# Performance work log

Hardware: AMD Instinct MI355X
Metric: run time of the kernel (lower is better)

The kernel has to match this reference:

```python
import jax, jax.numpy as jnp
import numpy as np

# segment-boundary byte set (matches ByteContextEncoder.SEGMENT_BYTES)
_SEG_BYTES = b' \t\n\r.,;:!?()[]{}"\'' + b'+-*/=<>|&^~%@#$\\'
_SEP_TABLE = np.zeros(256, dtype=bool)
_SEP_TABLE[list(_SEG_BYTES)] = True

B, T, D, H, L = 4, 2048, 512, 8, 4
HID = 4 * D          # SwiGLU hidden dim
DH = D // H          # head dim
EPS = 1e-6
ALPHA = 0.5
ROPE_BASE = 10000.0


def setup_inputs() -> dict:
    key = jax.random.key(0)
    ks = jax.random.split(key, 10)
    std = D ** -0.5
    tokens = jax.random.randint(ks[0], (B, T), 0, 256)
    embed = jax.random.normal(ks[1], (256, D), dtype=jnp.float32) * std
    wq = jax.random.normal(ks[2], (L, D, D), dtype=jnp.float32) * std
    wk = jax.random.normal(ks[3], (L, D, D), dtype=jnp.float32) * std
    wv = jax.random.normal(ks[4], (L, D, D), dtype=jnp.float32) * std
    wo = jax.random.normal(ks[5], (L, D, D), dtype=jnp.float32) * std
    w1 = jax.random.normal(ks[6], (L, HID, D), dtype=jnp.float32) * std  # gate proj
    w3 = jax.random.normal(ks[7], (L, HID, D), dtype=jnp.float32) * std  # up proj
    w2 = jax.random.normal(ks[8], (L, D, HID), dtype=jnp.float32) * (HID ** -0.5)  # down proj
    attn_norm_w = jnp.ones((L, D), dtype=jnp.float32)
    ffn_norm_w = jnp.ones((L, D), dtype=jnp.float32)
    final_norm_w = jnp.ones((D,), dtype=jnp.float32)
    return {"tokens": tokens, "embed": embed, "attn_norm_w": attn_norm_w,
            "wq": wq, "wk": wk, "wv": wv, "wo": wo,
            "ffn_norm_w": ffn_norm_w, "w1": w1, "w2": w2, "w3": w3,
            "final_norm_w": final_norm_w}


def _rmsnorm(x, w):
    return x * jax.lax.rsqrt(jnp.mean(x * x, axis=-1, keepdims=True) + EPS) * w


def _rope_tables():
    inv = 1.0 / (ROPE_BASE ** (jnp.arange(0, DH, 2, dtype=jnp.float32) / DH))  # (DH/2,)
    ang = jnp.arange(T, dtype=jnp.float32)[:, None] * inv[None, :]             # (T, DH/2)
    return jnp.cos(ang), jnp.sin(ang)


def _apply_rope(x, cos, sin):
    # x: (B, T, H, DH); rotate interleaved pairs
    x1, x2 = x[..., ::2], x[..., 1::2]
    c = cos[None, :, None, :]
    s = sin[None, :, None, :]
    r1 = x1 * c - x2 * s
    r2 = x1 * s + x2 * c
    return jnp.stack([r1, r2], axis=-1).reshape(x.shape)


def _attention(x, Wq, Wk, Wv, Wo, cos, sin):
    q = (x @ Wq.T).reshape(B, T, H, DH)
    k = (x @ Wk.T).reshape(B, T, H, DH)
    v = (x @ Wv.T).reshape(B, T, H, DH)
    q = _apply_rope(q, cos, sin)
    k = _apply_rope(k, cos, sin)
    scores = jnp.einsum('bthd,bshd->bhts', q, k) / jnp.sqrt(jnp.float32(DH))
    a = jax.nn.softmax(scores, axis=-1)  # bidirectional (causal=False)
    o = jnp.einsum('bhts,bshd->bthd', a, v).reshape(B, T, D)
    return o @ Wo.T


def _swiglu(x, W1, W2, W3):
    return (jax.nn.silu(x @ W1.T) * (x @ W3.T)) @ W2.T


def _segment_pool(h, tokens):
    # segment ids via cumsum of separator indicator; per-batch offset b*(T+1)
    sep = jnp.asarray(_SEP_TABLE)[tokens].astype(jnp.int32)          # (B, T)
    seg = jnp.cumsum(sep, axis=1) + jnp.arange(B, dtype=jnp.int32)[:, None] * (T + 1)
    flat_s = seg.reshape(B * T)
    flat_h = h.reshape(B * T, D)
    nseg = B * (T + 1)
    seg_sum = jax.ops.segment_sum(flat_h, flat_s, num_segments=nseg)  # (nseg, D)
    seg_cnt = jax.ops.segment_sum(jnp.ones((B * T,), h.dtype), flat_s, num_segments=nseg)
    seg_cnt = jnp.maximum(seg_cnt, 1.0)
    seg_mean = (seg_sum / seg_cnt[:, None])[flat_s].reshape(B, T, D)
    return ALPHA * h + (1.0 - ALPHA) * seg_mean


def reference(tokens, embed, attn_norm_w, wq, wk, wv, wo, ffn_norm_w, w1, w2, w3, final_norm_w):
    tokens = jnp.clip(tokens, 0, 255)
    x = embed[tokens]  # (B, T, D); dropout=0 -> identity
    cos, sin = _rope_tables()
    for l in range(L):
        x = x + _attention(_rmsnorm(x, attn_norm_w[l]), wq[l], wk[l], wv[l], wo[l], cos, sin)
        x = x + _swiglu(_rmsnorm(x, ffn_norm_w[l]), w1[l], w2[l], w3[l])
    x = _rmsnorm(x, final_norm_w)
    return _segment_pool(x, tokens)
```

## Files before the change

kernel.cpp:

```cpp
#include <hip/hip_runtime.h>
#include <math.h>

#define Bq 4
#define Tt 2048
#define Dd 512
#define Hh 8
#define Ll 4
#define HIDN 2048
#define DHd 64
#define BT (Bq*Tt)
#define BTD ((size_t)BT*Dd)

typedef __attribute__((ext_vector_type(8))) __bf16 bf16x8;
typedef __attribute__((ext_vector_type(4))) __bf16 bf16x4;
typedef __attribute__((ext_vector_type(2))) __bf16 bf16x2;
typedef __attribute__((ext_vector_type(4))) float f32x4;

static __device__ __forceinline__ int is_sep(int t) {
    const unsigned long long w0 = 0xFC00FFFF00002600ULL;
    const unsigned long long w1 = 0x7800000078000001ULL;
    if (t < 64)  return (int)((w0 >> t) & 1ULL);
    if (t < 128) return (int)((w1 >> (t - 64)) & 1ULL);
    return 0;
}

static __device__ __forceinline__ void gload16(const void* g, void* l) {
    __builtin_amdgcn_global_load_lds(
        (const __attribute__((address_space(1))) void*)g,
        (__attribute__((address_space(3))) void*)l, 16, 0, 0);
}

__global__ void embed_kernel(const int* __restrict__ tokens, const float* __restrict__ embed,
                             float* __restrict__ x) {
    size_t idx = (size_t)blockIdx.x * blockDim.x + threadIdx.x;
    if (idx >= BTD / 4) return;
    size_t row = idx >> 7;
    int tk = tokens[row];
    tk = tk < 0 ? 0 : (tk > 255 ? 255 : tk);
    const float4* src = (const float4*)(embed + (size_t)tk * Dd);
    ((float4*)x)[idx] = src[idx & 127];
}

__global__ void rope_table_kernel(float* __restrict__ cosb, float* __restrict__ sinb) {
    int idx = blockIdx.x * blockDim.x + threadIdx.x;
    if (idx >= Tt * 32) return;
    int t = idx >> 5, j = idx & 31;
    float inv = powf(10000.0f, -(2.0f * j) / 64.0f);
    float ang = (float)t * inv;
    cosb[idx] = cosf(ang);
    sinb[idx] = sinf(ang);
}

__global__ void cvt_bf16_kernel(const float* __restrict__ in, __bf16* __restrict__ out, int n8) {
    int i = blockIdx.x * blockDim.x + threadIdx.x;
    if (i >= n8) return;
    const float4* p = (const float4*)(in + (size_t)i * 8);
    float4 a = p[0], b = p[1];
    bf16x8 o8;
    o8[0] = (__bf16)a.x; o8[1] = (__bf16)a.y; o8[2] = (__bf16)a.z; o8[3] = (__bf16)a.w;
    o8[4] = (__bf16)b.x; o8[5] = (__bf16)b.y; o8[6] = (__bf16)b.z; o8[7] = (__bf16)b.w;
    *(bf16x8*)(out + (size_t)i * 8) = o8;
}

__global__ void cvt_qkv_kernel(const float* __restrict__ wq, const float* __restrict__ wk,
                               const float* __restrict__ wv, __bf16* __restrict__ out) {
    int i = blockIdx.x * blockDim.x + threadIdx.x;
    if (i >= 393216) return;
    int l = i / 98304;
    int r = i - l * 98304;
    int t = r >> 15;
    int pos8 = r & 32767;
    const float* src = (t == 0 ? wq : (t == 1 ? wk : wv)) + (size_t)l * 262144 + (size_t)pos8 * 8;
    float4 a = *(const float4*)src;
    float4 b = *(const float4*)(src + 4);
    bf16x8 o8;
    o8[0] = (__bf16)a.x; o8[1] = (__bf16)a.y; o8[2] = (__bf16)a.z; o8[3] = (__bf16)a.w;
    o8[4] = (__bf16)b.x; o8[5] = (__bf16)b.y; o8[6] = (__bf16)b.z; o8[7] = (__bf16)b.w;
    *(bf16x8*)(out + (size_t)i * 8) = o8;
}

__global__ void rmsnorm_kernel(const float* __restrict__ x, const float* __restrict__ w,
                               float* __restrict__ y) {
    int row = blockIdx.x * 4 + (threadIdx.x >> 6);
    int lane = threadIdx.x & 63;
    const float* xr = x + (size_t)row * Dd + lane * 8;
    float4 a = *(const float4*)xr;
    float4 b = *(const float4*)(xr + 4);
    float ss = a.x * a.x + a.y * a.y + a.z * a.z + a.w * a.w
             + b.x * b.x + b.y * b.y + b.z * b.z + b.w * b.w;
    #pragma unroll
    for (int off = 1; off < 64; off <<= 1) ss += __shfl_xor(ss, off);
    float scale = rsqrtf(ss * (1.0f / Dd) + 1e-6f);
    const float* wr = w + lane * 8;
    float4 wa = *(const float4*)wr;
    float4 wb = *(const float4*)(wr + 4);
    float* yo = y + (size_t)row * Dd + lane * 8;
    *(float4*)yo = make_float4(a.x * scale * wa.x, a.y * scale * wa.y,
                               a.z * scale * wa.z, a.w * scale * wa.w);
    *(float4*)(yo + 4) = make_float4(b.x * scale * wb.x, b.y * scale * wb.y,
                                     b.z * scale * wb.z, b.w * scale * wb.w);
}

__global__ void rmsnorm_bf16_kernel(const float* __restrict__ x, const float* __restrict__ w,
                                    __bf16* __restrict__ y) {
    int row = blockIdx.x * 4 + (threadIdx.x >> 6);
    int lane = threadIdx.x & 63;
    const float* xr = x + (size_t)row * Dd + lane * 8;
    float4 a = *(const float4*)xr;
    float4 b = *(const float4*)(xr + 4);
    float ss = a.x * a.x + a.y * a.y + a.z * a.z + a.w * a.w
             + b.x * b.x + b.y * b.y + b.z * b.z + b.w * b.w;
    #pragma unroll
    for (int off = 1; off < 64; off <<= 1) ss += __shfl_xor(ss, off);
    float scale = rsqrtf(ss * (1.0f / Dd) + 1e-6f);
    const float* wr = w + lane * 8;
    float4 wa = *(const float4*)wr;
    float4 wb = *(const float4*)(wr + 4);
    bf16x8 o;
    o[0] = (__bf16)(a.x * scale * wa.x); o[1] = (__bf16)(a.y * scale * wa.y);
    o[2] = (__bf16)(a.z * scale * wa.z); o[3] = (__bf16)(a.w * scale * wa.w);
    o[4] = (__bf16)(b.x * scale * wb.x); o[5] = (__bf16)(b.y * scale * wb.y);
    o[6] = (__bf16)(b.z * scale * wb.z); o[7] = (__bf16)(b.w * scale * wb.w);
    *(bf16x8*)(y + (size_t)row * Dd + lane * 8) = o;
}

template<int EPI>
__global__ __launch_bounds__(256) void gemm_bt_mfma(
    const __bf16* __restrict__ A, const __bf16* __restrict__ Bw,
    const float* __restrict__ res, void* __restrict__ Cout,
    int N, int K,
    const float* __restrict__ cosb, const float* __restrict__ sinb) {
    __shared__ __align__(16) __bf16 lds[2][2][128 * 32];
    const int tid = threadIdx.x;
    const int w = tid >> 6, lane = tid & 63;
    const int l15 = lane & 15, g4 = lane >> 4;
    const int wr = w >> 1, wc = w & 1;
    const int bm = blockIdx.y * 128, bn = blockIdx.x * 128;
    const int lrow = lane >> 2, lc8 = (lane & 3) * 8;
    const int chunk0 = w * 2;

    f32x4 acc[4][4];
    #pragma unroll
    for (int m = 0; m < 4; m++)
        #pragma unroll
        for (int n = 0; n < 4; n++) acc[m][n] = (f32x4){0.f, 0.f, 0.f, 0.f};

    auto stage = [&](int buf, int k0) {
        #pragma unroll
        for (int c = 0; c < 2; c++) {
            int chunk = chunk0 + c;
            const __bf16* ga = A + (size_t)(bm + chunk * 16 + lrow) * K + k0 + lc8;
            gload16(ga, &lds[buf][0][chunk * 512]);
            const __bf16* gb = Bw + (size_t)(bn + chunk * 16 + lrow) * K + k0 + lc8;
            gload16(gb, &lds[buf][1][chunk * 512]);
        }
    };

    stage(0, 0);
    __syncthreads();
    const int NT = K >> 5;
    int cur = 0;
    for (int t = 0; t < NT; t++) {
        if (t + 1 < NT) stage(cur ^ 1, (t + 1) << 5);
        const __bf16* Al = &lds[cur][0][0];
        const __bf16* Bl = &lds[cur][1][0];
        bf16x8 af[4], bfr[4];
        #pragma unroll
        for (int m = 0; m < 4; m++)
            af[m] = *(const bf16x8*)&Al[(wr * 64 + m * 16 + l15) * 32 + g4 * 8];
        #pragma unroll
        for (int n = 0; n < 4; n++)
            bfr[n] = *(const bf16x8*)&Bl[(wc * 64 + n * 16 + l15) * 32 + g4 * 8];
        #pragma unroll
        for (int m = 0; m < 4; m++)
            #pragma unroll
            for (int n = 0; n < 4; n++)
                acc[m][n] = __builtin_amdgcn_mfma_f32_16x16x32_bf16(af[m], bfr[n], acc[m][n], 0, 0, 0);
        __syncthreads();
        cur ^= 1;
    }

    #pragma unroll
    for (int m = 0; m < 4; m++)
        #pragma unroll
        for (int n = 0; n < 4; n++)
            #pragma unroll
            for (int r = 0; r < 4; r++) {
                size_t row = bm + wr * 64 + m * 16 + g4 * 4 + r;
                int col = bn + wc * 64 + n * 16 + l15;
                if (EPI == 0) {
                    ((__bf16*)Cout)[row * N + col] = (__bf16)acc[m][n][r];
                } else if (EPI == 1) {
                    ((float*)Cout)[row * N + col] = acc[m][n][r] + res[row * N + col];
                } else {
                    float vv = acc[m][n][r];
                    float vp = __shfl_xor(vv, 1);
                    if (col < 1024) {
                        int trow = (int)(row & (Tt - 1));
                        int p = (col & 63) >> 1;
                        float c = cosb[trow * 32 + p];
                        float s = sinb[trow * 32 + p];
                        float x1 = (col & 1) ? vp : vv;
                        float x2 = (col & 1) ? vv : vp;
                        float rot = (col & 1) ? (x1 * s + x2 * c) : (x1 * c - x2 * s);
                        if (col < 512) rot *= 0.18033688011112043f;
                        vv = rot;
                    }
                    ((__bf16*)Cout)[(size_t)(col >> 9) * BTD + row * 512 + (col & 511)] =
                        (__bf16)vv;
                }
            }
}

__global__ __launch_bounds__(256) void gemm_bt_mfma64(
    const __bf16* __restrict__ A, const __bf16* __restrict__ Bw,
    const float* __restrict__ res, float* __restrict__ Cout,
    int N, int K) {
    __shared__ __align__(16) __bf16 lds[2][2][64 * 32];
    const int tid = threadIdx.x;
    const int w = tid >> 6, lane = tid & 63;
    const int l15 = lane & 15, g4 = lane >> 4;
    const int wr = w >> 1, wc = w & 1;
    const int bm = blockIdx.y * 64, bn = blockIdx.x * 64;
    const int srow = tid >> 2, scol8 = (tid & 3) * 8;

    f32x4 acc[2][2];
    #pragma unroll
    for (int m = 0; m < 2; m++)
        #pragma unroll
        for (int n = 0; n < 2; n++) acc[m][n] = (f32x4){0.f, 0.f, 0.f, 0.f};

    auto stage = [&](int buf, int k0) {
        gload16(A + (size_t)(bm + srow) * K + k0 + scol8, &lds[buf][0][srow * 32 + scol8]);
        gload16(Bw + (size_t)(bn + srow) * K + k0 + scol8, &lds[buf][1][srow * 32 + scol8]);
    };

    stage(0, 0);
    __syncthreads();
    const int NT = K >> 5;
    int cur = 0;
    for (int t = 0; t < NT; t++) {
        if (t + 1 < NT) stage(cur ^ 1, (t + 1) << 5);
        const __bf16* Al = &lds[cur][0][0];
        const __bf16* Bl = &lds[cur][1][0];
        bf16x8 af[2], bfr[2];
        #pragma unroll
        for (int m = 0; m < 2; m++)
            af[m] = *(const bf16x8*)&Al[(wr * 32 + m * 16 + l15) * 32 + g4 * 8];
        #pragma unroll
        for (int n = 0; n < 2; n++)
            bfr[n] = *(const bf16x8*)&Bl[(wc * 32 + n * 16 + l15) * 32 + g4 * 8];
        #pragma unroll
        for (int m = 0; m < 2; m++)
            #pragma unroll
            for (int n = 0; n < 2; n++)
                acc[m][n] = __builtin_amdgcn_mfma_f32_16x16x32_bf16(af[m], bfr[n], acc[m][n], 0, 0, 0);
        __syncthreads();
        cur ^= 1;
    }

    #pragma unroll
    for (int m = 0; m < 2; m++)
        #pragma unroll
        for (int n = 0; n < 2; n++)
            #pragma unroll
            for (int r = 0; r < 4; r++) {
                size_t row = bm + wr * 32 + m * 16 + g4 * 4 + r;
                int col = bn + wc * 32 + n * 16 + l15;
                Cout[row * N + col] = acc[m][n][r] + res[row * N + col];
            }
}

__global__ __launch_bounds__(256) void gemm_swiglu_mfma(
    const __bf16* __restrict__ A, const __bf16* __restrict__ W1,
    const __bf16* __restrict__ W3, __bf16* __restrict__ G,
    int N, int K) {
    __shared__ __align__(16) __bf16 lds[2][3][128 * 32];
    const int tid = threadIdx.x;
    const int w = tid >> 6, lane = tid & 63;
    const int l15 = lane & 15, g4 = lane >> 4;
    const int wr = w >> 1, wc = w & 1;
    const int bm = blockIdx.y * 128, bn = blockIdx.x * 128;
    const int lrow = lane >> 2, lc8 = (lane & 3) * 8;
    const int chunk0 = w * 2;

    f32x4 acc1[4][4], acc3[4][4];
    #pragma unroll
    for (int m = 0; m < 4; m++)
        #pragma unroll
        for (int n = 0; n < 4; n++) {
            acc1[m][n] = (f32x4){0.f, 0.f, 0.f, 0.f};
            acc3[m][n] = (f32x4){0.f, 0.f, 0.f, 0.f};
        }

    auto stage = [&](int buf, int k0) {
        #pragma unroll
        for (int c = 0; c < 2; c++) {
            int chunk = chunk0 + c;
            const __bf16* ga = A + (size_t)(bm + chunk * 16 + lrow) * K + k0 + lc8;
            gload16(ga, &lds[buf][0][chunk * 512]);
            const __bf16* g1 = W1 + (size_t)(bn + chunk * 16 + lrow) * K + k0 + lc8;
            gload16(g1, &lds[buf][1][chunk * 512]);
            const __bf16* g3 = W3 + (size_t)(bn + chunk * 16 + lrow) * K + k0 + lc8;
            gload16(g3, &lds[buf][2][chunk * 512]);
        }
    };

    stage(0, 0);
    __syncthreads();
    const int NT = K >> 5;
    int cur = 0;
    for (int t = 0; t < NT; t++) {
        if (t + 1 < NT) stage(cur ^ 1, (t + 1) << 5);
        const __bf16* Al = &lds[cur][0][0];
        const __bf16* B1 = &lds[cur][1][0];
        const __bf16* B3 = &lds[cur][2][0];
        bf16x8 af[4];
        #pragma unroll
        for (int m = 0; m < 4; m++)
            af[m] = *(const bf16x8*)&Al[(wr * 64 + m * 16 + l15) * 32 + g4 * 8];
        #pragma unroll
        for (int n = 0; n < 4; n++) {
            bf16x8 b1 = *(const bf16x8*)&B1[(wc * 64 + n * 16 + l15) * 32 + g4 * 8];
            bf16x8 b3 = *(const bf16x8*)&B3[(wc * 64 + n * 16 + l15) * 32 + g4 * 8];
            #pragma unroll
            for (int m = 0; m < 4; m++) {
                acc1[m][n] = __builtin_amdgcn_mfma_f32_16x16x32_bf16(af[m], b1, acc1[m][n], 0, 0, 0);
                acc3[m][n] = __builtin_amdgcn_mfma_f32_16x16x32_bf16(af[m], b3, acc3[m][n], 0, 0, 0);
            }
        }
        __syncthreads();
        cur ^= 1;
    }

    #pragma unroll
    for (int m = 0; m < 4; m++)
        #pragma unroll
        for (int n = 0; n < 4; n++)
            #pragma unroll
            for (int r = 0; r < 4; r++) {
                size_t row = bm + wr * 64 + m * 16 + g4 * 4 + r;
                size_t col = bn + wc * 64 + n * 16 + l15;
                float a1 = acc1[m][n][r];
                float sig = 1.0f / (1.0f + __expf(-a1));
                G[row * N + col] = (__bf16)(a1 * sig * acc3[m][n][r]);
            }
}

__global__ __launch_bounds__(256) void attn_mfma_kernel(
    const __bf16* __restrict__ q, const __bf16* __restrict__ k,
    const __bf16* __restrict__ v, __bf16* __restrict__ o) {
    __shared__ __align__(16) __bf16 Ks[64][72];
    __shared__ __align__(16) unsigned int VtW[64 * 36];
    __shared__ __align__(16) __bf16 Ps[4][16][72];

    int tid = threadIdx.x;
    int w = tid >> 6;
    int lane = tid & 63;
    int l15 = lane & 15;
    int g = lane >> 4;
    int i = blockIdx.x;
    int xcd = i & 7, jj = i >> 3;
    int bh = xcd * 4 + (jj >> 5);
    int qtile = jj & 31;
    int b = bh >> 3, h = bh & 7;
    int qbase = qtile * 64;

    const __bf16* qp = q + (size_t)b * Tt * Dd + (size_t)h * DHd;
    const __bf16* kp = k + (size_t)b * Tt * Dd + (size_t)h * DHd;
    const __bf16* vp = v + (size_t)b * Tt * Dd + (size_t)h * DHd;

    int r2 = tid >> 3;
    int sc8 = (tid & 7) * 8;

    bf16x8 qa[2];
    {
        const __bf16* qrow = qp + (size_t)(qbase + w * 16 + l15) * Dd;
        qa[0] = *(const bf16x8*)(qrow + g * 8);
        qa[1] = *(const bf16x8*)(qrow + 32 + g * 8);
    }

    f32x4 oacc[4];
    #pragma unroll
    for (int i2 = 0; i2 < 4; i2++) oacc[i2] = (f32x4){0.f, 0.f, 0.f, 0.f};
    float mrun[4] = {-1e30f, -1e30f, -1e30f, -1e30f};
    float lrun[4] = {0.f, 0.f, 0.f, 0.f};

    bf16x8 kreg[2], vreg[2];
    auto ldkv = [&](int t) {
        size_t base = (size_t)(t * 64) * Dd;
        kreg[0] = *(const bf16x8*)(kp + base + (size_t)r2 * Dd + sc8);
        kreg[1] = *(const bf16x8*)(kp + base + (size_t)(r2 + 32) * Dd + sc8);
        vreg[0] = *(const bf16x8*)(vp + base + (size_t)(2 * r2) * Dd + sc8);
        vreg[1] = *(const bf16x8*)(vp + base + (size_t)(2 * r2 + 1) * Dd + sc8);
    };

    ldkv(0);
    const int NT = Tt / 64;
    for (int t = 0; t < NT; t++) {
        __syncthreads();
        *(bf16x8*)&Ks[r2][sc8] = kreg[0];
        *(bf16x8*)&Ks[r2 + 32][sc8] = kreg[1];
        {
            const unsigned short* v0 = (const unsigned short*)&vreg[0];
            const unsigned short* v1 = (const unsigned short*)&vreg[1];
            #pragma unroll
            for (int j = 0; j < 8; j++) {
                int d = sc8 + j;
                int col = (r2 + 4 * ((d >> 3) & 7)) & 31;
                unsigned int word = (unsigned int)v0[j] | ((unsigned int)v1[j] << 16);
                VtW[d * 36 + col] = word;
            }
        }
        if (t + 1 < NT) ldkv(t + 1);
        __syncthreads();

        f32x4 s4[4];
        __builtin_amdgcn_s_setprio(1);
        #pragma unroll
        for (int c = 0; c < 4; c++) {
            s4[c] = (f32x4){0.f, 0.f, 0.f, 0.f};
            bf16x8 kb0 = *(const bf16x8*)&Ks[c * 16 + l15][g * 8];
            s4[c] = __builtin_amdgcn_mfma_f32_16x16x32_bf16(qa[0], kb0, s4[c], 0, 0, 0);
            bf16x8 kb1 = *(const bf16x8*)&Ks[c * 16 + l15][32 + g * 8];
            s4[c] = __builtin_amdgcn_mfma_f32_16x16x32_bf16(qa[1], kb1, s4[c], 0, 0, 0);
        }
        __builtin_amdgcn_s_setprio(0);

        float lm[4];
        #pragma unroll
        for (int r = 0; r < 4; r++)
            lm[r] = fmaxf(fmaxf(s4[0][r], s4[1][r]), fmaxf(s4[2][r], s4[3][r]));
        bool near = (lm[0] - mrun[0] <= 8.f) && (lm[1] - mrun[1] <= 8.f)
                 && (lm[2] - mrun[2] <= 8.f) && (lm[3] - mrun[3] <= 8.f);
        if (!__all((int)near)) {
            float alpha[4];
            #pragma unroll
            for (int r = 0; r < 4; r++) {
                float tm = lm[r];
                #pragma unroll
                for (int off = 1; off < 16; off <<= 1)
                    tm = fmaxf(tm, __shfl_xor(tm, off));
                float mnew = fmaxf(mrun[r], tm);
                alpha[r] = exp2f(mrun[r] - mnew);
                mrun[r] = mnew;
            }
            #pragma unroll
            for (int r = 0; r < 4; r++) lrun[r] *= alpha[r];
            #pragma unroll
            for (int d2 = 0; d2 < 4; d2++)
                #pragma unroll
                for (int r = 0; r < 4; r++) oacc[d2][r] *= alpha[r];
        }
        float plane[4] = {0.f, 0.f, 0.f, 0.f};
        #pragma unroll
        for (int c = 0; c < 4; c++)
            #pragma unroll
            for (int r = 0; r < 4; r++) {
                float e = exp2f(s4[c][r] - mrun[r]);
                s4[c][r] = e;
                plane[r] += e;
            }
        #pragma unroll
        for (int r = 0; r < 4; r++) lrun[r] += plane[r];
        #pragma unroll
        for (int c = 0; c < 4; c++)
            #pragma unroll
            for (int r = 0; r < 4; r++)
                Ps[w][g * 4 + r][c * 16 + l15] = (__bf16)s4[c][r];

        bf16x8 pa0 = *(const bf16x8*)&Ps[w][l15][g * 8];
        bf16x8 pa1 = *(const bf16x8*)&Ps[w][l15][32 + g * 8];
        __builtin_amdgcn_s_setprio(1);
        #pragma unroll
        for (int d2 = 0; d2 < 4; d2++) {
            int d = d2 * 16 + l15;
            int rot = ((2 * d2 + (l15 >> 3)) & 7) * 4;
            const unsigned int* vrow = VtW + d * 36;
            bf16x8 vb0 = *(const bf16x8*)(vrow + ((4 * g + rot) & 31));
            bf16x8 vb1 = *(const bf16x8*)(vrow + ((16 + 4 * g + rot) & 31));
            oacc[d2] = __builtin_amdgcn_mfma_f32_16x16x32_bf16(pa0, vb0, oacc[d2], 0, 0, 0);
            oacc[d2] = __builtin_amdgcn_mfma_f32_16x16x32_bf16(pa1, vb1, oacc[d2], 0, 0, 0);
        }
        __builtin_amdgcn_s_setprio(0);
    }

    #pragma unroll
    for (int r = 0; r < 4; r++) {
        #pragma unroll
        for (int off = 1; off < 16; off <<= 1)
            lrun[r] += __shfl_xor(lrun[r], off);
    }

    __bf16* op = o + (size_t)b * Tt * Dd + (size_t)h * DHd;
    #pragma unroll
    for (int d2 = 0; d2 < 4; d2++)
        #pragma unroll
        for (int r = 0; r < 4; r++)
            op[(size_t)(qbase + w * 16 + g * 4 + r) * Dd + d2 * 16 + l15] =
                (__bf16)(oacc[d2][r] / lrun[r]);
}

__global__ void seg_scan_kernel(const int* __restrict__ tokens, int* __restrict__ segid) {
    int b = blockIdx.x;
    int tid = threadIdx.x;
    const int* trow = tokens + (size_t)b * Tt;
    int base = tid * 8;
    int inc[8];
    int run = 0;
    #pragma unroll
    for (int i = 0; i < 8; i++) {
        int tk = trow[base + i];
        tk = tk < 0 ? 0 : (tk > 255 ? 255 : tk);
        run += is_sep(tk);
        inc[i] = run;
    }
    __shared__ int part[256];
    part[tid] = run;
    __syncthreads();
    for (int off = 1; off < 256; off <<= 1) {
        int vv = (tid >= off) ? part[tid - off] : 0;
        __syncthreads();
        part[tid] += vv;
        __syncthreads();
    }
    int exc = part[tid] - run;
    #pragma unroll
    for (int i = 0; i < 8; i++)
        segid[(size_t)b * Tt + base + i] = exc + inc[i] + b * (Tt + 1);
}

__global__ void seg_cnt_kernel(const int* __restrict__ segid, float* __restrict__ cnt) {
    int i = blockIdx.x * blockDim.x + threadIdx.x;
    if (i < BT) atomicAdd(&cnt[segid[i]], 1.0f);
}

__global__ void seg_accum_kernel(const float* __restrict__ h, const int* __restrict__ segid,
                                 float* __restrict__ segsum) {
    size_t idx = (size_t)blockIdx.x * blockDim.x + threadIdx.x;
    if (idx >= BTD) return;
    size_t row = idx >> 9;
    int d = idx & 511;
    atomicAdd(&segsum[(size_t)segid[row] * Dd + d], h[idx]);
}

__global__ void seg_final_kernel(const float* __restrict__ h, const float* __restrict__ segsum,
                                 const float* __restrict__ cnt, const int* __restrict__ segid,
                                 float* __restrict__ out) {
    size_t idx = (size_t)blockIdx.x * blockDim.x + threadIdx.x;
    if (idx >= BTD) return;
    size_t row = idx >> 9;
    int d = idx & 511;
    int s = segid[row];
    float mean = segsum[(size_t)s * Dd + d] / fmaxf(cnt[s], 1.0f);
    out[idx] = 0.5f * h[idx] + 0.5f * mean;
}

extern "C" void kernel_launch(void* const* d_in, const int* in_sizes, int n_in,
                              void* d_out, int out_size, void* d_ws, size_t ws_size,
                              hipStream_t stream) {
    const int*   tokens       = (const int*)d_in[0];
    const float* embedw       = (const float*)d_in[1];
    const float* attn_norm_w  = (const float*)d_in[2];
    const float* wq           = (const float*)d_in[3];
    const float* wk           = (const float*)d_in[4];
    const float* wv           = (const float*)d_in[5];
    const float* wo           = (const float*)d_in[6];
    const float* ffn_norm_w   = (const float*)d_in[7];
    const float* w1           = (const float*)d_in[8];
    const float* w2           = (const float*)d_in[9];
    const float* w3           = (const float*)d_in[10];
    const float* final_norm_w = (const float*)d_in[11];
    float* out = (float*)d_out;
    float* ws  = (float*)d_ws;

    float*  x    = ws;
    __bf16* qkvo = (__bf16*)(ws + BTD);
    __bf16* qb   = qkvo;
    __bf16* kb   = qkvo + BTD;
    __bf16* vb   = qkvo + 2 * BTD;
    __bf16* obuf = qkvo + 3 * BTD;
    __bf16* gbuf = qkvo;
    float*  segsum = ws;
    float*  hfin   = ws + 2 * BTD;
    __bf16* xnb  = (__bf16*)(ws + 3 * BTD);
    __bf16* wb   = (__bf16*)(ws + 3 * BTD + BTD / 2);
    float*  cosb = ws + 3 * BTD + BTD / 2 + 8388608;
    float*  sinb = cosb + (size_t)Tt * 32;
    float*  segcnt = sinb + (size_t)Tt * 32;
    int*    segid  = (int*)(segcnt + Bq * (Tt + 1));

    __bf16* wqkvb = wb;
    __bf16* wob = wb + 3145728;
    __bf16* w1b = wb + 4194304;
    __bf16* w3b = wb + 8388608;
    __bf16* w2b = wb + 12582912;

    cvt_qkv_kernel<<<1536, 256, 0, stream>>>(wq, wk, wv, wqkvb);
    cvt_bf16_kernel<<<512, 256, 0, stream>>>(wo, wob, 131072);
    cvt_bf16_kernel<<<2048, 256, 0, stream>>>(w1, w1b, 524288);
    cvt_bf16_kernel<<<2048, 256, 0, stream>>>(w3, w3b, 524288);
    cvt_bf16_kernel<<<2048, 256, 0, stream>>>(w2, w2b, 524288);

    embed_kernel<<<(int)((BTD / 4 + 255) / 256), 256, 0, stream>>>(tokens, embedw, x);
    rope_table_kernel<<<(Tt * 32 + 255) / 256, 256, 0, stream>>>(cosb, sinb);

    dim3 gqkv(12, 64);
    dim3 g64(8, 128);
    dim3 gs(16, 64);
    dim3 ga(1024);
    int grms = BT / 4;

    for (int l = 0; l < Ll; l++) {
        size_t oDD = (size_t)l * Dd * Dd;
        size_t oHD = (size_t)l * HIDN * Dd;
        rmsnorm_bf16_kernel<<<grms, 256, 0, stream>>>(x, attn_norm_w + (size_t)l * Dd, xnb);
        gemm_bt_mfma<2><<<gqkv, 256, 0, stream>>>(xnb, wqkvb + (size_t)l * 786432, nullptr, qb,
                                                  1536, Dd, cosb, sinb);
        attn_mfma_kernel<<<ga, 256, 0, stream>>>(qb, kb, vb, obuf);
        gemm_bt_mfma64<<<g64, 256, 0, stream>>>(obuf, wob + oDD, x, x, Dd, Dd);
        rmsnorm_bf16_kernel<<<grms, 256, 0, stream>>>(x, ffn_norm_w + (size_t)l * Dd, xnb);
        gemm_swiglu_mfma<<<gs, 256, 0, stream>>>(xnb, w1b + oHD, w3b + oHD, gbuf, HIDN, Dd);
        gemm_bt_mfma64<<<g64, 256, 0, stream>>>(gbuf, w2b + oHD, x, x, Dd, HIDN);
    }

    rmsnorm_kernel<<<grms, 256, 0, stream>>>(x, final_norm_w, hfin);

    hipMemsetAsync(segsum, 0, (size_t)Bq * (Tt + 1) * Dd * sizeof(float), stream);
    hipMemsetAsync(segcnt, 0, (size_t)Bq * (Tt + 1) * sizeof(float), stream);
    seg_scan_kernel<<<Bq, 256, 0, stream>>>(tokens, segid);
    seg_cnt_kernel<<<(BT + 255) / 256, 256, 0, stream>>>(segid, segcnt);
    seg_accum_kernel<<<(int)((BTD + 255) / 256), 256, 0, stream>>>(hfin, segid, segsum);
    seg_final_kernel<<<(int)((BTD + 255) / 256), 256, 0, stream>>>(hfin, segsum, segcnt, segid, out);
}
```

Baseline: 1.067 ms.

## Compute transposed S in attention to keep P in registers, dropping LDS round-trip

The QK^T MFMA now swaps its operands to produce S^T with a permuted key-row mapping. Each lane then holds one query's scores across keys in a layout that can be packed straight into the A operand of the PV MFMA. This removes the per-tile P shared-memory write/read and per-row shuffle reductions, since softmax stats become per-lane scalars. The cost is a few cross-lane shuffles to remap alpha and the final normalizer back to the O-accumulator layout, plus reliance on a subtle register-layout correspondence.

```diff
diff --git a/kernel.cpp b/kernel.cpp
--- a/kernel.cpp
+++ b/kernel.cpp
@@ -352,7 +352,6 @@
     const __bf16* __restrict__ v, __bf16* __restrict__ o) {
     __shared__ __align__(16) __bf16 Ks[64][72];
     __shared__ __align__(16) unsigned int VtW[64 * 36];
-    __shared__ __align__(16) __bf16 Ps[4][16][72];
 
     int tid = threadIdx.x;
     int w = tid >> 6;
@@ -372,6 +371,7 @@
 
     int r2 = tid >> 3;
     int sc8 = (tid & 7) * 8;
+    int sgrow = 8 * (l15 >> 2) + (l15 & 3);
 
     bf16x8 qa[2];
     {
@@ -383,8 +383,8 @@
     f32x4 oacc[4];
     #pragma unroll
     for (int i2 = 0; i2 < 4; i2++) oacc[i2] = (f32x4){0.f, 0.f, 0.f, 0.f};
-    float mrun[4] = {-1e30f, -1e30f, -1e30f, -1e30f};
-    float lrun[4] = {0.f, 0.f, 0.f, 0.f};
+    float mrun = -1e30f;
+    float lrun = 0.f;
 
     bf16x8 kreg[2], vreg[2];
     auto ldkv = [&](int t) {
@@ -419,58 +419,49 @@
         __builtin_amdgcn_s_setprio(1);
         #pragma unroll
         for (int c = 0; c < 4; c++) {
+            int row = sgrow + (c & 1) * 32 + (c >> 1) * 4;
             s4[c] = (f32x4){0.f, 0.f, 0.f, 0.f};
-            bf16x8 kb0 = *(const bf16x8*)&Ks[c * 16 + l15][g * 8];
-            s4[c] = __builtin_amdgcn_mfma_f32_16x16x32_bf16(qa[0], kb0, s4[c], 0, 0, 0);
-            bf16x8 kb1 = *(const bf16x8*)&Ks[c * 16 + l15][32 + g * 8];
-            s4[c] = __builtin_amdgcn_mfma_f32_16x16x32_bf16(qa[1], kb1, s4[c], 0, 0, 0);
+            bf16x8 kb0 = *(const bf16x8*)&Ks[row][g * 8];
+            s4[c] = __builtin_amdgcn_mfma_f32_16x16x32_bf16(kb0, qa[0], s4[c], 0, 0, 0);
+            bf16x8 kb1 = *(const bf16x8*)&Ks[row][32 + g * 8];
+            s4[c] = __builtin_amdgcn_mfma_f32_16x16x32_bf16(kb1, qa[1], s4[c], 0, 0, 0);
         }
         __builtin_amdgcn_s_setprio(0);
 
-        float lm[4];
-        #pragma unroll
-        for (int r = 0; r < 4; r++)
-            lm[r] = fmaxf(fmaxf(s4[0][r], s4[1][r]), fmaxf(s4[2][r], s4[3][r]));
-        bool near = (lm[0] - mrun[0] <= 8.f) && (lm[1] - mrun[1] <= 8.f)
-                 && (lm[2] - mrun[2] <= 8.f) && (lm[3] - mrun[3] <= 8.f);
+        float lm = fmaxf(fmaxf(fmaxf(s4[0][0], s4[0][1]), fmaxf(s4[0][2], s4[0][3])),
+                         fmaxf(fmaxf(s4[1][0], s4[1][1]), fmaxf(s4[1][2], s4[1][3])));
+        lm = fmaxf(lm, fmaxf(fmaxf(s4[2][0], s4[2][1]), fmaxf(s4[2][2], s4[2][3])));
+        lm = fmaxf(lm, fmaxf(fmaxf(s4[3][0], s4[3][1]), fmaxf(s4[3][2], s4[3][3])));
+        bool near = (lm - mrun <= 8.f);
         if (!__all((int)near)) {
-            float alpha[4];
-            #pragma unroll
-            for (int r = 0; r < 4; r++) {
-                float tm = lm[r];
-                #pragma unroll
-                for (int off = 1; off < 16; off <<= 1)
-                    tm = fmaxf(tm, __shfl_xor(tm, off));
-                float mnew = fmaxf(mrun[r], tm);
-                alpha[r] = exp2f(mrun[r] - mnew);
-                mrun[r] = mnew;
-            }
-            #pragma unroll
-            for (int r = 0; r < 4; r++) lrun[r] *= alpha[r];
+            float tm = fmaxf(lm, __shfl_xor(lm, 16));
+            tm = fmaxf(tm, __shfl_xor(tm, 32));
+            float mnew = fmaxf(mrun, tm);
+            float alpha = exp2f(mrun - mnew);
+            mrun = mnew;
+            lrun *= alpha;
+            float ar[4];
+            #pragma unroll
+            for (int r = 0; r < 4; r++) ar[r] = __shfl(alpha, 20 * g + r);
             #pragma unroll
             for (int d2 = 0; d2 < 4; d2++)
                 #pragma unroll
-                for (int r = 0; r < 4; r++) oacc[d2][r] *= alpha[r];
-        }
-        float plane[4] = {0.f, 0.f, 0.f, 0.f};
-        #pragma unroll
-        for (int c = 0; c < 4; c++)
+                for (int r = 0; r < 4; r++) oacc[d2][r] *= ar[r];
+        }
+        float psum = 0.f;
+        bf16x8 pa0, pa1;
+        #pragma unroll
+        for (int cc = 0; cc < 2; cc++)
             #pragma unroll
             for (int r = 0; r < 4; r++) {
-                float e = exp2f(s4[c][r] - mrun[r]);
-                s4[c][r] = e;
-                plane[r] += e;
+                float e0 = exp2f(s4[2 * cc][r] - mrun);
+                float e1 = exp2f(s4[2 * cc + 1][r] - mrun);
+                psum += e0 + e1;
+                pa0[cc * 4 + r] = (__bf16)e0;
+                pa1[cc * 4 + r] = (__bf16)e1;
             }
-        #pragma unroll
-        for (int r = 0; r < 4; r++) lrun[r] += plane[r];
-        #pragma unroll
-        for (int c = 0; c < 4; c++)
-            #pragma unroll
-            for (int r = 0; r < 4; r++)
-                Ps[w][g * 4 + r][c * 16 + l15] = (__bf16)s4[c][r];
-
-        bf16x8 pa0 = *(const bf16x8*)&Ps[w][l15][g * 8];
-        bf16x8 pa1 = *(const bf16x8*)&Ps[w][l15][32 + g * 8];
+        lrun += psum;
+
         __builtin_amdgcn_s_setprio(1);
         #pragma unroll
         for (int d2 = 0; d2 < 4; d2++) {
@@ -485,12 +476,11 @@
         __builtin_amdgcn_s_setprio(0);
     }
 
-    #pragma unroll
-    for (int r = 0; r < 4; r++) {
-        #pragma unroll
-        for (int off = 1; off < 16; off <<= 1)
-            lrun[r] += __shfl_xor(lrun[r], off);
-    }
+    lrun += __shfl_xor(lrun, 16);
+    lrun += __shfl_xor(lrun, 32);
+    float lr[4];
+    #pragma unroll
+    for (int r = 0; r < 4; r++) lr[r] = __shfl(lrun, 20 * g + r);
 
     __bf16* op = o + (size_t)b * Tt * Dd + (size_t)h * DHd;
     #pragma unroll
@@ -498,7 +488,7 @@
         #pragma unroll
         for (int r = 0; r < 4; r++)
             op[(size_t)(qbase + w * 16 + g * 4 + r) * Dd + d2 * 16 + l15] =
-                (__bf16)(oacc[d2][r] / lrun[r]);
+                (__bf16)(oacc[d2][r] / lr[r]);
 }
 
 __global__ void seg_scan_kernel(const int* __restrict__ tokens, int* __restrict__ segid) {
```

Result: faster. 1.014 ms (median of 3 runs) (-5.0%).
